# Optimization experiments

Measured on AMD Instinct MI355X. Metric: run time of the kernel, lower is better.

Reference implementation:

```python
import jax, jax.numpy as jnp
import numpy as np

B, P, K, L, F_NR, KS, NC = 32, 2048, 16, 8, 64, 5, 40
N = B * P
EPS = 1e-5


def setup_inputs() -> dict:
    key = jax.random.key(0)
    ks = jax.random.split(key, 6)
    pos = jax.random.normal(ks[0], (N, 3), jnp.float32)
    batch = jnp.repeat(jnp.arange(B, dtype=jnp.int32), P)
    # SplineConv(1, F_NR, dim=3, kernel_size=KS): weight [KS^3, in=1, out] flattened to [KS^3, F]
    w_spline = jax.random.normal(ks[1], (KS ** 3, F_NR), jnp.float32) * 0.1
    w_root = jax.random.normal(ks[2], (F_NR,), jnp.float32) * 0.1
    b_spline = jnp.zeros((F_NR,), jnp.float32)
    bn_gamma = jnp.ones((F_NR,), jnp.float32)
    bn_beta = jnp.zeros((F_NR,), jnp.float32)
    w1 = jax.random.normal(ks[3], (F_NR, 256), jnp.float32) / np.sqrt(F_NR).astype(np.float32)
    b1 = jnp.zeros((256,), jnp.float32)
    w2 = jax.random.normal(ks[4], (256, NC), jnp.float32) / np.sqrt(256).astype(np.float32)
    b2 = jnp.zeros((NC,), jnp.float32)
    return dict(pos=pos, batch=batch, w_spline=w_spline, w_root=w_root,
                b_spline=b_spline, bn_gamma=bn_gamma, bn_beta=bn_beta,
                w1=w1, b1=b1, w2=w2, b2=b2)


def _knn_one_cloud(pb):  # pb: [P,3] -> k nearest neighbor indices [P,K] (no self loops)
    sq = jnp.sum(pb * pb, axis=-1)
    d = sq[:, None] + sq[None, :] - 2.0 * (pb @ pb.T)
    d = jnp.where(jnp.eye(P, dtype=bool), jnp.inf, d)
    _, idx = jax.lax.top_k(-d, K)
    return idx


def reference(pos, batch, w_spline, w_root, b_spline, bn_gamma, bn_beta, w1, b1, w2, b2):
    # --- knn_graph, grouped k-per-center ---
    posb = pos.reshape(B, P, 3)
    nbr = jax.vmap(_knn_one_cloud)(posb)                          # [B,P,K] local
    nbr = (nbr + (jnp.arange(B) * P)[:, None, None]).reshape(N, K)
    clusters = pos[nbr] - pos[:, None, :]                          # [N,K,3]
    # --- per-point 3x3 covariance over first L neighbors ---
    cl = clusters[:, :L, :]
    cov = jnp.einsum('nlc,nld->ncd', cl, cl)                       # [N,3,3]
    # --- diag(): 5 iterations of batched QR iteration; rows of V = eigenvectors ---
    A = cov
    Vt = jnp.broadcast_to(jnp.eye(3, dtype=pos.dtype), (N, 3, 3))
    for _ in range(5):
        Q, R = jnp.linalg.qr(A)
        A = R @ Q
        Vt = Vt @ Q
    V = jnp.swapaxes(Vt, 1, 2)                                     # [N,3,3]
    # --- rotate clusters into eigenbasis: clusters @ V^T ---
    dc = jnp.einsum('nkc,ndc->nkd', clusters, V)                   # [N,K,3]
    signs = jnp.sign(jnp.sum(dc[:, :, 2], axis=1))
    dc = dc.at[:, :, 2].multiply(signs[:, None])
    max_abs = jnp.max(jnp.abs(dc).reshape(N, K * 3), axis=1)
    dc = dc / max_abs[:, None, None] * 0.5 + 0.5                   # pseudo coords in [0,1]
    # --- SplineConv (degree-1 open B-splines, dim=3): x_j = 1, aggr='mean' ---
    p = dc * (KS - 1)
    i0 = jnp.clip(jnp.floor(p), 0, KS - 2).astype(jnp.int32)       # [N,K,3]
    f = p - i0                                                     # fractional part
    acc = jnp.zeros((N, K, F_NR), pos.dtype)
    for c in range(8):                                             # 8 corners of trilinear basis
        bits = [(c >> d) & 1 for d in range(3)]
        kidx = sum((i0[..., d] + bits[d]) * (KS ** d) for d in range(3))
        w = jnp.ones((N, K), pos.dtype)
        for d in range(3):
            w = w * (f[..., d] if bits[d] else 1.0 - f[..., d])
        acc = acc + w[..., None] * w_spline[kidx]                  # [N,K,F]
    out_nondir = acc.mean(axis=1) + w_root + b_spline              # root*x_i + bias, x_i = 1
    # --- BatchNorm1d (training-mode batch stats, biased var) ---
    mu = out_nondir.mean(axis=0)
    var = out_nondir.var(axis=0)
    y = (out_nondir - mu) / jnp.sqrt(var + EPS) * bn_gamma + bn_beta
    # --- head ---
    y = jax.nn.sigmoid(y)
    ys = y.reshape(B, P, F_NR).mean(axis=1)                        # [B,F]
    y1 = jax.nn.elu(ys @ w1 + b1)
    y2 = jax.nn.log_softmax(y1 @ w2 + b2, axis=1)
    return y2
```

## Files before the change

kernel.cpp:

```cpp
#include <hip/hip_runtime.h>
#include <math.h>

#define B_ 32
#define P_ 2048
#define N_ 65536
#define K_ 16
#define L_ 8
#define F_ 64
#define KS_ 5
#define KS3_ 125
#define NC_ 40
#define H_ 256
#define EPS_ 1e-5f
#define QPB_ 64
#define SEG_ 4

__device__ __forceinline__ float distf(float4 C, float nx, float ny, float nz, float qs) {
    return fmaf(C.x, nx, fmaf(C.y, ny, fmaf(C.z, nz, C.w))) + qs;
}

#define CES(a, b) { unsigned _mn = min(a, b); b = max(a, b); a = _mn; }

__device__ __forceinline__ void sort8(unsigned& e0, unsigned& e1, unsigned& e2, unsigned& e3,
                                      unsigned& e4, unsigned& e5, unsigned& e6, unsigned& e7) {
    CES(e0, e1) CES(e2, e3) CES(e4, e5) CES(e6, e7)
    CES(e0, e2) CES(e1, e3) CES(e4, e6) CES(e5, e7)
    CES(e1, e2) CES(e5, e6)
    CES(e0, e4) CES(e1, e5) CES(e2, e6) CES(e3, e7)
    CES(e2, e4) CES(e3, e5)
    CES(e1, e2) CES(e3, e4) CES(e5, e6)
}

__device__ __forceinline__ void bitmerge16(unsigned (&a)[16]) {
#pragma unroll
    for (int dd = 8; dd >= 1; dd >>= 1)
#pragma unroll
        for (int k2 = 0; k2 < 16; k2 += 2 * dd)
#pragma unroll
            for (int i2 = k2; i2 < k2 + dd; i2++)
                CES(a[i2], a[i2 + dd])
}

__device__ __forceinline__ void sort16(unsigned (&a)[16]) {
    sort8(a[0], a[1], a[2], a[3], a[4], a[5], a[6], a[7]);
    sort8(a[8], a[9], a[10], a[11], a[12], a[13], a[14], a[15]);
    unsigned t;
    t = a[8];  a[8]  = a[15]; a[15] = t;
    t = a[9];  a[9]  = a[14]; a[14] = t;
    t = a[10]; a[10] = a[13]; a[13] = t;
    t = a[11]; a[11] = a[12]; a[12] = t;
    bitmerge16(a);
}

__device__ __forceinline__ void flush8(unsigned (&bu)[16],
                                       unsigned& e0, unsigned& e1, unsigned& e2, unsigned& e3,
                                       unsigned& e4, unsigned& e5, unsigned& e6, unsigned& e7,
                                       unsigned& thr) {
    sort8(e0, e1, e2, e3, e4, e5, e6, e7);
    CES(bu[8],  e7) CES(bu[9],  e6) CES(bu[10], e5) CES(bu[11], e4)
    CES(bu[12], e3) CES(bu[13], e2) CES(bu[14], e1) CES(bu[15], e0)
    bitmerge16(bu);
    e0 = e1 = e2 = e3 = e4 = e5 = e6 = e7 = 0xFFFFFFFFu;
    unsigned t16 = bu[15];
    t16 = min(t16, (unsigned)__shfl_xor((int)t16, 1, 64));
    t16 = min(t16, (unsigned)__shfl_xor((int)t16, 2, 64));
    thr = min(thr, t16);
}

__global__ __launch_bounds__(256, 2) void knn_geom_kernel(const float* __restrict__ pos,
                                                          float* __restrict__ dcn) {
    __shared__ float4 cloud[P_ + 8];
    int b = blockIdx.x >> 5, tile = blockIdx.x & 31;
    int base = b * P_;
    int t = threadIdx.x;
    for (int j = t; j < P_; j += 256) {
        float x = pos[(base + j) * 3 + 0];
        float y = pos[(base + j) * 3 + 1];
        float z = pos[(base + j) * 3 + 2];
        cloud[j] = make_float4(x, y, z, x * x + y * y + z * z);
    }
    if (t < 8) cloud[P_ + t] = make_float4(0.f, 0.f, 0.f, 1e30f);
    __syncthreads();

    int s = t & 3;
    int il = tile * QPB_ + (t >> 2);
    float4 Q = cloud[il];
    float nx = -2.f * Q.x, ny = -2.f * Q.y, nz = -2.f * Q.z, qs = Q.w;

    int j0 = s << 9, off = s << 1;

    unsigned bu[16];
#pragma unroll
    for (int m = 0; m < 16; m++) {
        int j_ = j0 + off + m;
        float4 Cv = cloud[j_];
        float d_ = distf(Cv, nx, ny, nz, qs);
        bu[m] = (__float_as_uint(fmaxf(d_, 0.f)) & 0xFFFFF800u) | (unsigned)j_;
    }
    sort16(bu);
    unsigned thr;
    {
        unsigned t16 = bu[15];
        t16 = min(t16, (unsigned)__shfl_xor((int)t16, 1, 64));
        t16 = min(t16, (unsigned)__shfl_xor((int)t16, 2, 64));
        thr = t16;
    }

    unsigned e0 = ~0u, e1 = ~0u, e2 = ~0u, e3 = ~0u,
             e4 = ~0u, e5 = ~0u, e6 = ~0u, e7 = ~0u;

#define VISITL(Cv, Jv) {                                                         \
        float d_ = distf(Cv, nx, ny, nz, qs);                                    \
        unsigned key_ = (__float_as_uint(fmaxf(d_, 0.f)) & 0xFFFFF800u)          \
                        | (unsigned)(Jv);                                        \
        bool a_ = (key_ < thr);                                                  \
        e7 = a_ ? e6 : e7;  e6 = a_ ? e5 : e6;  e5 = a_ ? e4 : e5;               \
        e4 = a_ ? e3 : e4;  e3 = a_ ? e2 : e3;  e2 = a_ ? e1 : e2;               \
        e1 = a_ ? e0 : e1;  e0 = a_ ? key_ : e0;                                 \
    }
#define VISITP(Cv, Jv, P) {                                                      \
        float d_ = distf(Cv, nx, ny, nz, qs);                                    \
        unsigned key_ = (__float_as_uint(fmaxf(d_, 0.f)) & 0xFFFFF800u)          \
                        | (unsigned)(Jv);                                        \
        bool a_ = (key_ < thr) && (P);                                           \
        e7 = a_ ? e6 : e7;  e6 = a_ ? e5 : e6;  e5 = a_ ? e4 : e5;               \
        e4 = a_ ? e3 : e4;  e3 = a_ ? e2 : e3;  e2 = a_ ? e1 : e2;               \
        e1 = a_ ? e0 : e1;  e0 = a_ ? key_ : e0;                                 \
    }

    const float4* cp = &cloud[j0 + off + 16];
    int jc = j0 + off + 16;
    for (int v = 0; v < 488; v += 4) {
        float4 a0 = cp[v + 0], a1 = cp[v + 1], a2 = cp[v + 2], a3 = cp[v + 3];
        VISITL(a0, jc + 0)
        VISITL(a1, jc + 1)
        VISITL(a2, jc + 2)
        VISITL(a3, jc + 3)
        jc += 4;
        if (__any(e4 != 0xFFFFFFFFu))
            flush8(bu, e0, e1, e2, e3, e4, e5, e6, e7, thr);
    }
    {
        int vlim = 496 - off;
#pragma unroll
        for (int v = 488; v < 492; v++) {
            float4 a0 = cp[v];
            VISITP(a0, jc, v < vlim) jc++;
        }
        if (__any(e4 != 0xFFFFFFFFu))
            flush8(bu, e0, e1, e2, e3, e4, e5, e6, e7, thr);
#pragma unroll
        for (int v = 492; v < 496; v++) {
            float4 a0 = cp[v];
            VISITP(a0, jc, v < vlim) jc++;
        }
        if (__any(e4 != 0xFFFFFFFFu))
            flush8(bu, e0, e1, e2, e3, e4, e5, e6, e7, thr);
    }
    {
#pragma unroll
        for (int u = 0; u < 4; u++) {
            float4 a0 = cloud[j0 + u];
            VISITP(a0, j0 + u, u < off)
        }
        if (__any(e4 != 0xFFFFFFFFu))
            flush8(bu, e0, e1, e2, e3, e4, e5, e6, e7, thr);
#pragma unroll
        for (int u = 4; u < 6; u++) {
            float4 a0 = cloud[j0 + u];
            VISITP(a0, j0 + u, u < off)
        }
    }
    flush8(bu, e0, e1, e2, e3, e4, e5, e6, e7, thr);
#undef VISITL
#undef VISITP

    {
        bool own = (s == (il >> 9));
#pragma unroll
        for (int m = 0; m < 15; m++) bu[m] = own ? bu[m + 1] : bu[m];
        bu[15] = own ? 0xFFFFFFFFu : bu[15];
    }

#pragma unroll
    for (int mask = 1; mask <= 2; mask <<= 1) {
        unsigned o[16];
#pragma unroll
        for (int i = 0; i < 16; i++)
            o[i] = (unsigned)__shfl_xor((int)bu[15 - i], mask, 64);
#pragma unroll
        for (int i = 0; i < 16; i++) bu[i] = min(bu[i], o[i]);
        bitmerge16(bu);
    }

    float px = Q.x, py = Q.y, pz = Q.z;
    float A[3][3];
    {
        float a00 = 0, a01 = 0, a02 = 0, a11 = 0, a12 = 0, a22 = 0;
#pragma unroll
        for (int l = 0; l < L_; l++) {
            float4 Cv = cloud[bu[l] & 0x7FF];
            float ccx = Cv.x - px, ccy = Cv.y - py, ccz = Cv.z - pz;
            a00 += ccx * ccx; a01 += ccx * ccy; a02 += ccx * ccz;
            a11 += ccy * ccy; a12 += ccy * ccz; a22 += ccz * ccz;
        }
        A[0][0] = a00; A[0][1] = a01; A[0][2] = a02;
        A[1][0] = a01; A[1][1] = a11; A[1][2] = a12;
        A[2][0] = a02; A[2][1] = a12; A[2][2] = a22;
    }
    float Vt[3][3] = {{1.f, 0.f, 0.f}, {0.f, 1.f, 0.f}, {0.f, 0.f, 1.f}};

    for (int it = 0; it < 5; it++) {
        float M00 = A[0][0], M01 = A[0][1], M02 = A[0][2];
        float M10 = A[1][0], M11 = A[1][1], M12 = A[1][2];
        float M20 = A[2][0], M21 = A[2][1], M22 = A[2][2];
        float tau0 = 0.f, v1 = 0.f, v2 = 0.f;
        float xn2 = M10 * M10 + M20 * M20;
        if (xn2 != 0.f) {
            float beta = -copysignf(sqrtf(M00 * M00 + xn2), M00);
            tau0 = (beta - M00) / beta;
            float inv = 1.f / (M00 - beta);
            v1 = M10 * inv; v2 = M20 * inv;
            float sc;
            sc = tau0 * (M01 + v1 * M11 + v2 * M21); M01 -= sc; M11 -= v1 * sc; M21 -= v2 * sc;
            sc = tau0 * (M02 + v1 * M12 + v2 * M22); M02 -= sc; M12 -= v1 * sc; M22 -= v2 * sc;
            M00 = beta;
        }
        float tau1 = 0.f, u2 = 0.f;
        if (M21 != 0.f) {
            float beta1 = -copysignf(sqrtf(M11 * M11 + M21 * M21), M11);
            tau1 = (beta1 - M11) / beta1;
            u2 = M21 / (M11 - beta1);
            float sc = tau1 * (M12 + u2 * M22); M12 -= sc; M22 -= u2 * sc;
            M11 = beta1;
        }
        float h11 = 1.f - tau1, h12 = -tau1 * u2, h22 = 1.f - tau1 * u2 * u2;
        float Qm[3][3];
        Qm[0][0] = 1.f - tau0;
        Qm[1][0] = -v1 * tau0;
        Qm[2][0] = -v2 * tau0;
        float t1 = tau0 * (v1 * h11 + v2 * h12);
        Qm[0][1] = -t1;
        Qm[1][1] = h11 - v1 * t1;
        Qm[2][1] = h12 - v2 * t1;
        float t2 = tau0 * (v1 * h12 + v2 * h22);
        Qm[0][2] = -t2;
        Qm[1][2] = h12 - v1 * t2;
        Qm[2][2] = h22 - v2 * t2;
        A[0][0] = M00 * Qm[0][0] + M01 * Qm[1][0] + M02 * Qm[2][0];
        A[0][1] = M00 * Qm[0][1] + M01 * Qm[1][1] + M02 * Qm[2][1];
        A[0][2] = M00 * Qm[0][2] + M01 * Qm[1][2] + M02 * Qm[2][2];
        A[1][0] = M11 * Qm[1][0] + M12 * Qm[2][0];
        A[1][1] = M11 * Qm[1][1] + M12 * Qm[2][1];
        A[1][2] = M11 * Qm[1][2] + M12 * Qm[2][2];
        A[2][0] = M22 * Qm[2][0];
        A[2][1] = M22 * Qm[2][1];
        A[2][2] = M22 * Qm[2][2];
        float nv[3][3];
#pragma unroll
        for (int r = 0; r < 3; r++)
#pragma unroll
            for (int cc = 0; cc < 3; cc++)
                nv[r][cc] = Vt[r][0] * Qm[0][cc] + Vt[r][1] * Qm[1][cc] + Vt[r][2] * Qm[2][cc];
#pragma unroll
        for (int r = 0; r < 3; r++)
#pragma unroll
            for (int cc = 0; cc < 3; cc++) Vt[r][cc] = nv[r][cc];
    }

    float s2 = 0.f, mx01 = 0.f, mx2 = 0.f;
#pragma unroll
    for (int k = 0; k < K_; k++) {
        float4 Cv = cloud[bu[k] & 0x7FF];
        float ccx = Cv.x - px, ccy = Cv.y - py, ccz = Cv.z - pz;
        float d0 = ccx * Vt[0][0] + ccy * Vt[1][0] + ccz * Vt[2][0];
        float d1 = ccx * Vt[0][1] + ccy * Vt[1][1] + ccz * Vt[2][1];
        float d2 = ccx * Vt[0][2] + ccy * Vt[1][2] + ccz * Vt[2][2];
        s2 += d2;
        mx01 = fmaxf(mx01, fmaxf(fabsf(d0), fabsf(d1)));
        mx2  = fmaxf(mx2, fabsf(d2));
    }
    float sg = (s2 > 0.f) ? 1.f : ((s2 < 0.f) ? -1.f : 0.f);
    float mx = fmaxf(mx01, (sg == 0.f) ? 0.f : mx2);
    float hs = 0.5f / mx;

    {
        int i = base + il;
        float4* row = (float4*)(dcn + (size_t)i * 48);
        bool od = (s & 1) != 0, hi = (s & 2) != 0;
        unsigned lo0 = od ? bu[4]  : bu[0],  hi0 = od ? bu[12] : bu[8];
        unsigned lo1 = od ? bu[5]  : bu[1],  hi1 = od ? bu[13] : bu[9];
        unsigned lo2 = od ? bu[6]  : bu[2],  hi2 = od ? bu[14] : bu[10];
        unsigned lo3 = od ? bu[7]  : bu[3],  hi3 = od ? bu[15] : bu[11];
        unsigned u0 = hi ? hi0 : lo0;
        unsigned u1 = hi ? hi1 : lo1;
        unsigned u2 = hi ? hi2 : lo2;
        unsigned u3 = hi ? hi3 : lo3;
        float v[12];
        float4 Cv;
        Cv = cloud[u0 & 0x7FF];
        {
            float ccx = Cv.x - px, ccy = Cv.y - py, ccz = Cv.z - pz;
            float d2 = (ccx * Vt[0][2] + ccy * Vt[1][2] + ccz * Vt[2][2]) * sg;
            v[0] = (ccx * Vt[0][0] + ccy * Vt[1][0] + ccz * Vt[2][0]) * hs + 0.5f;
            v[1] = (ccx * Vt[0][1] + ccy * Vt[1][1] + ccz * Vt[2][1]) * hs + 0.5f;
            v[2] = d2 * hs + 0.5f;
        }
        Cv = cloud[u1 & 0x7FF];
        {
            float ccx = Cv.x - px, ccy = Cv.y - py, ccz = Cv.z - pz;
            float d2 = (ccx * Vt[0][2] + ccy * Vt[1][2] + ccz * Vt[2][2]) * sg;
            v[3] = (ccx * Vt[0][0] + ccy * Vt[1][0] + ccz * Vt[2][0]) * hs + 0.5f;
            v[4] = (ccx * Vt[0][1] + ccy * Vt[1][1] + ccz * Vt[2][1]) * hs + 0.5f;
            v[5] = d2 * hs + 0.5f;
        }
        Cv = cloud[u2 & 0x7FF];
        {
            float ccx = Cv.x - px, ccy = Cv.y - py, ccz = Cv.z - pz;
            float d2 = (ccx * Vt[0][2] + ccy * Vt[1][2] + ccz * Vt[2][2]) * sg;
            v[6] = (ccx * Vt[0][0] + ccy * Vt[1][0] + ccz * Vt[2][0]) * hs + 0.5f;
            v[7] = (ccx * Vt[0][1] + ccy * Vt[1][1] + ccz * Vt[2][1]) * hs + 0.5f;
            v[8] = d2 * hs + 0.5f;
        }
        Cv = cloud[u3 & 0x7FF];
        {
            float ccx = Cv.x - px, ccy = Cv.y - py, ccz = Cv.z - pz;
            float d2 = (ccx * Vt[0][2] + ccy * Vt[1][2] + ccz * Vt[2][2]) * sg;
            v[9]  = (ccx * Vt[0][0] + ccy * Vt[1][0] + ccz * Vt[2][0]) * hs + 0.5f;
            v[10] = (ccx * Vt[0][1] + ccy * Vt[1][1] + ccz * Vt[2][1]) * hs + 0.5f;
            v[11] = d2 * hs + 0.5f;
        }
        row[s * 3 + 0] = make_float4(v[0], v[1], v[2], v[3]);
        row[s * 3 + 1] = make_float4(v[4], v[5], v[6], v[7]);
        row[s * 3 + 2] = make_float4(v[8], v[9], v[10], v[11]);
    }
}

__global__ __launch_bounds__(256) void spline_kernel(const float* __restrict__ dcn,
                                                     const float* __restrict__ w_spline,
                                                     const float* __restrict__ w_root,
                                                     const float* __restrict__ b_spline,
                                                     float* __restrict__ x,
                                                     float* __restrict__ partials) {
    __shared__ float ws_t[F_ * KS3_];
    __shared__ float red[4][64];
    {
        int f = threadIdx.x & 63;
        for (int c = threadIdx.x >> 6; c < KS3_; c += 4)
            ws_t[f * KS3_ + c] = w_spline[c * 64 + f];
    }
    __syncthreads();
    int wave = threadIdx.x >> 6, f = threadIdx.x & 63;
    const float* wbase = &ws_t[f * KS3_];
    float wr = w_root[f] + b_spline[f];
    float s1 = 0.f, s2 = 0.f;
    for (int p = 0; p < 16; p++) {
        int i = blockIdx.x * 64 + wave * 16 + p;
        const float4* row = (const float4*)(dcn + (size_t)i * 48);
        float pr[48];
#pragma unroll
        for (int m = 0; m < 12; m++) {
            float4 v = row[m];
            pr[m * 4 + 0] = v.x; pr[m * 4 + 1] = v.y;
            pr[m * 4 + 2] = v.z; pr[m * 4 + 3] = v.w;
        }
        float acc = 0.f;
#pragma unroll
        for (int k = 0; k < K_; k++) {
            float p0 = pr[k * 3 + 0] * 4.f;
            float p1 = pr[k * 3 + 1] * 4.f;
            float p2 = pr[k * 3 + 2] * 4.f;
            float i0 = fminf(fmaxf(floorf(p0), 0.f), 3.f);
            float i1 = fminf(fmaxf(floorf(p1), 0.f), 3.f);
            float i2 = fminf(fmaxf(floorf(p2), 0.f), 3.f);
            float f0 = p0 - i0, f1 = p1 - i1, f2 = p2 - i2;
            float g0 = 1.f - f0, g1 = 1.f - f1, g2 = 1.f - f2;
            int c = (int)fmaf(i2, 25.f, fmaf(i1, 5.f, i0));
            const float* wp = wbase + c;
            float a0 = wp[0],  a1 = wp[1];
            float b0 = wp[5],  b1v = wp[6];
            float c0 = wp[25], c1 = wp[26];
            float d0 = wp[30], d1 = wp[31];
            float wA = g1 * g2, wB = f1 * g2, wC = g1 * f2, wD = f1 * f2;
            acc = fmaf(wA, fmaf(f0, a1, g0 * a0), acc);
            acc = fmaf(wB, fmaf(f0, b1v, g0 * b0), acc);
            acc = fmaf(wC, fmaf(f0, c1, g0 * c0), acc);
            acc = fmaf(wD, fmaf(f0, d1, g0 * d0), acc);
        }
        float xv = acc * (1.f / 16.f) + wr;
        x[(size_t)i * 64 + f] = xv;
        s1 += xv; s2 += xv * xv;
    }
    red[wave][f] = s1; __syncthreads();
    if (threadIdx.x < 64)
        partials[blockIdx.x * 128 + f] = red[0][f] + red[1][f] + red[2][f] + red[3][f];
    __syncthreads();
    red[wave][f] = s2; __syncthreads();
    if (threadIdx.x < 64)
        partials[blockIdx.x * 128 + 64 + f] = red[0][f] + red[1][f] + red[2][f] + red[3][f];
}

__global__ __launch_bounds__(256) void stats_kernel(const float* __restrict__ partials,
                                                    const float* __restrict__ gamma,
                                                    const float* __restrict__ beta,
                                                    float* __restrict__ stats) {
    __shared__ double red1[256], red2[256];
    int t = threadIdx.x;
    int f = t & 63, g = t >> 6;
    double a0 = 0, a1 = 0, a2 = 0, a3 = 0, q0 = 0, q1 = 0, q2 = 0, q3 = 0;
    for (int b2 = g; b2 < 1024; b2 += 16) {
        a0 += (double)partials[(b2     ) * 128 + f];
        q0 += (double)partials[(b2     ) * 128 + 64 + f];
        a1 += (double)partials[(b2 +  4) * 128 + f];
        q1 += (double)partials[(b2 +  4) * 128 + 64 + f];
        a2 += (double)partials[(b2 +  8) * 128 + f];
        q2 += (double)partials[(b2 +  8) * 128 + 64 + f];
        a3 += (double)partials[(b2 + 12) * 128 + f];
        q3 += (double)partials[(b2 + 12) * 128 + 64 + f];
    }
    red1[t] = (a0 + a1) + (a2 + a3);
    red2[t] = (q0 + q1) + (q2 + q3);
    __syncthreads();
    if (t < 64) {
        double S1 = red1[t] + red1[t + 64] + red1[t + 128] + red1[t + 192];
        double S2 = red2[t] + red2[t + 64] + red2[t + 128] + red2[t + 192];
        double mu = S1 / (double)N_;
        double var = S2 / (double)N_ - mu * mu;
        double scale = (double)gamma[t] / sqrt(var + (double)EPS_);
        double shift = (double)beta[t] - mu * scale;
        stats[t] = (float)scale;
        stats[64 + t] = (float)shift;
    }
}

__global__ __launch_bounds__(256) void pool_partial_kernel(const float* __restrict__ x,
                                                           const float* __restrict__ stats,
                                                           float* __restrict__ pp) {
    __shared__ float red[4][64];
    int blk = blockIdx.x;
    int b = blk >> 5, ch = blk & 31;
    int f = threadIdx.x & 63, w = threadIdx.x >> 6;
    float scale = stats[f], shift = stats[64 + f];
    float acc = 0.f;
    int row0 = b * P_ + ch * 64;
    for (int r = w; r < 64; r += 4) {
        float v = x[(size_t)(row0 + r) * 64 + f];
        float t = fmaf(v, scale, shift);
        acc += __fdividef(1.f, 1.f + __expf(-t));
    }
    red[w][f] = acc; __syncthreads();
    if (threadIdx.x < 64) pp[blk * 64 + f] = red[0][f] + red[1][f] + red[2][f] + red[3][f];
}

__global__ __launch_bounds__(256) void mlp_kernel(const float* __restrict__ pp,
                                                  const float* __restrict__ w1,
                                                  const float* __restrict__ b1,
                                                  const float* __restrict__ w2,
                                                  const float* __restrict__ b2,
                                                  float* __restrict__ out) {
    __shared__ float ssy[64];
    __shared__ float sy1[256];
    int b = blockIdx.x, t = threadIdx.x;
    if (t < 64) {
        float s = 0.f;
#pragma unroll
        for (int g = 0; g < 32; g++) s += pp[(b * 32 + g) * 64 + t];
        ssy[t] = s * (1.f / 2048.f);
    }
    __syncthreads();
    {
        float acc = b1[t];
#pragma unroll 8
        for (int c = 0; c < F_; c++) acc = fmaf(ssy[c], w1[c * 256 + t], acc);
        sy1[t] = acc > 0.f ? acc : expm1f(acc);
    }
    __syncthreads();
    if (t < 64) {
        int j = t;
        float acc = -INFINITY;
        if (j < NC_) {
            acc = b2[j];
#pragma unroll 8
            for (int c = 0; c < H_; c++) acc = fmaf(sy1[c], w2[c * 40 + j], acc);
        }
        float m = acc;
#pragma unroll
        for (int o = 32; o > 0; o >>= 1) m = fmaxf(m, __shfl_xor(m, o, 64));
        float e = (j < NC_) ? expf(acc - m) : 0.f;
        float s = e;
#pragma unroll
        for (int o = 32; o > 0; o >>= 1) s += __shfl_xor(s, o, 64);
        if (j < NC_) out[b * NC_ + j] = acc - m - logf(s);
    }
}

extern "C" void kernel_launch(void* const* d_in, const int* in_sizes, int n_in,
                              void* d_out, int out_size, void* d_ws, size_t ws_size,
                              hipStream_t stream) {
    const float* pos      = (const float*)d_in[0];
    const float* w_spline = (const float*)d_in[2];
    const float* w_root   = (const float*)d_in[3];
    const float* b_spline = (const float*)d_in[4];
    const float* bn_gamma = (const float*)d_in[5];
    const float* bn_beta  = (const float*)d_in[6];
    const float* w1       = (const float*)d_in[7];
    const float* b1       = (const float*)d_in[8];
    const float* w2       = (const float*)d_in[9];
    const float* b2       = (const float*)d_in[10];
    float* out = (float*)d_out;

    char* ws = (char*)d_ws;
    float* dcn      = (float*)(ws + 0);
    float* x        = (float*)(ws + (12u << 20));
    float* partials = (float*)(ws + (28u << 20));
    float* stats    = (float*)(ws + (28u << 20) + (512u << 10));
    float* pp       = (float*)(ws + (28u << 20) + (512u << 10) + 4096);

    knn_geom_kernel<<<B_ * 32, 256, 0, stream>>>(pos, dcn);
    spline_kernel<<<N_ / 64, 256, 0, stream>>>(dcn, w_spline, w_root, b_spline, x, partials);
    stats_kernel<<<1, 256, 0, stream>>>(partials, bn_gamma, bn_beta, stats);
    pool_partial_kernel<<<B_ * 32, 256, 0, stream>>>(x, stats, pp);
    mlp_kernel<<<B_, 256, 0, stream>>>(pp, w1, b1, w2, b2, out);
}
```

Measured before the change: 194.1 us.

## Store spline weight corners pre-expanded as fp16 for single vector LDS load

The spline kernel now stages, for each feature and each of the 64 base cells, the 8 trilinear corner weights contiguously in shared memory as fp16. Each neighbor then needs one 16-byte LDS read instead of eight scalar reads. The interpolation is refactored to nested lerps and the clamp uses fmed3. This trades fp16 precision on the weights for fewer LDS instructions, and the expanded table uses about 66KB of shared memory, which may lower occupancy.

After: 218.6 us. 1.13x slower.

```diff
diff --git a/kernel.cpp b/kernel.cpp
--- a/kernel.cpp
+++ b/kernel.cpp
@@ -1,4 +1,5 @@
 #include <hip/hip_runtime.h>
+#include <hip/hip_fp16.h>
 #include <math.h>
 
 #define B_ 32
@@ -342,16 +343,22 @@
                                                      const float* __restrict__ b_spline,
                                                      float* __restrict__ x,
                                                      float* __restrict__ partials) {
-    __shared__ float ws_t[F_ * KS3_];
+    __shared__ __half exp_h[F_ * 520];
     __shared__ float red[4][64];
-    {
-        int f = threadIdx.x & 63;
-        for (int c = threadIdx.x >> 6; c < KS3_; c += 4)
-            ws_t[f * KS3_ + c] = w_spline[c * 64 + f];
+    for (int idx = threadIdx.x; idx < 64 * 64; idx += 256) {
+        int f = idx & 63, bb = idx >> 6;
+        int i0 = bb & 3, i1 = (bb >> 2) & 3, i2 = bb >> 4;
+        const float* wp = w_spline + (i0 + 5 * i1 + 25 * i2) * 64 + f;
+        __half2 h0 = __float22half2_rn(make_float2(wp[0 * 64],  wp[1 * 64]));
+        __half2 h1 = __float22half2_rn(make_float2(wp[5 * 64],  wp[6 * 64]));
+        __half2 h2 = __float22half2_rn(make_float2(wp[25 * 64], wp[26 * 64]));
+        __half2 h3 = __float22half2_rn(make_float2(wp[30 * 64], wp[31 * 64]));
+        __half2* dst = (__half2*)&exp_h[f * 520 + bb * 8];
+        dst[0] = h0; dst[1] = h1; dst[2] = h2; dst[3] = h3;
     }
     __syncthreads();
     int wave = threadIdx.x >> 6, f = threadIdx.x & 63;
-    const float* wbase = &ws_t[f * KS3_];
+    const __half* exp_row = &exp_h[f * 520];
     float wr = w_root[f] + b_spline[f];
     float s1 = 0.f, s2 = 0.f;
     for (int p = 0; p < 16; p++) {
@@ -370,22 +377,25 @@
             float p0 = pr[k * 3 + 0] * 4.f;
             float p1 = pr[k * 3 + 1] * 4.f;
             float p2 = pr[k * 3 + 2] * 4.f;
-            float i0 = fminf(fmaxf(floorf(p0), 0.f), 3.f);
-            float i1 = fminf(fmaxf(floorf(p1), 0.f), 3.f);
-            float i2 = fminf(fmaxf(floorf(p2), 0.f), 3.f);
+            float i0 = __builtin_amdgcn_fmed3f(floorf(p0), 0.f, 3.f);
+            float i1 = __builtin_amdgcn_fmed3f(floorf(p1), 0.f, 3.f);
+            float i2 = __builtin_amdgcn_fmed3f(floorf(p2), 0.f, 3.f);
             float f0 = p0 - i0, f1 = p1 - i1, f2 = p2 - i2;
             float g0 = 1.f - f0, g1 = 1.f - f1, g2 = 1.f - f2;
-            int c = (int)fmaf(i2, 25.f, fmaf(i1, 5.f, i0));
-            const float* wp = wbase + c;
-            float a0 = wp[0],  a1 = wp[1];
-            float b0 = wp[5],  b1v = wp[6];
-            float c0 = wp[25], c1 = wp[26];
-            float d0 = wp[30], d1 = wp[31];
-            float wA = g1 * g2, wB = f1 * g2, wC = g1 * f2, wD = f1 * f2;
-            acc = fmaf(wA, fmaf(f0, a1, g0 * a0), acc);
-            acc = fmaf(wB, fmaf(f0, b1v, g0 * b0), acc);
-            acc = fmaf(wC, fmaf(f0, c1, g0 * c0), acc);
-            acc = fmaf(wD, fmaf(f0, d1, g0 * d0), acc);
+            int bb = (int)fmaf(i2, 16.f, fmaf(i1, 4.f, i0));
+            uint4 rv = *((const uint4*)(exp_row + bb * 8));
+            float2 cA = __half22float2(*(__half2*)&rv.x);
+            float2 cB = __half22float2(*(__half2*)&rv.y);
+            float2 cC = __half22float2(*(__half2*)&rv.z);
+            float2 cD = __half22float2(*(__half2*)&rv.w);
+            float Av = fmaf(f0, cA.y, g0 * cA.x);
+            float Bv = fmaf(f0, cB.y, g0 * cB.x);
+            float Cv = fmaf(f0, cC.y, g0 * cC.x);
+            float Dv = fmaf(f0, cD.y, g0 * cD.x);
+            float U = fmaf(f1, Bv, g1 * Av);
+            float V = fmaf(f1, Dv, g1 * Cv);
+            acc = fmaf(g2, U, acc);
+            acc = fmaf(f2, V, acc);
         }
         float xv = acc * (1.f / 16.f) + wr;
         x[(size_t)i * 64 + f] = xv;
```

## Restructure spline conv as scatter to dense coefficients then fp16 dot2 matmul

Applied to the files above, without the earlier changes.

The spline kernel now builds, per point, a dense 125-entry trilinear coefficient vector in shared memory by atomically accumulating the 8 corner weights of each of the 16 neighbours. That vector is packed to fp16 and multiplied against fp16-packed spline weights held in registers using dot2 instructions. This replaces the per-feature, per-neighbour gather and interpolation loop, which repeated the interpolation weights across all 64 features. In exchange it adds fp16 rounding of both weights and coefficients, LDS atomics, a large register array for the weights, and drops the lower clamp on the floor index.

Result: slower. 204.2 us (+5.2%).

```diff
diff --git a/kernel.cpp b/kernel.cpp
--- a/kernel.cpp
+++ b/kernel.cpp
@@ -14,6 +14,23 @@
 #define EPS_ 1e-5f
 #define QPB_ 64
 #define SEG_ 4
+
+typedef _Float16 h2v __attribute__((ext_vector_type(2)));
+
+__device__ __forceinline__ h2v u2h(unsigned u) { h2v h; __builtin_memcpy(&h, &u, 4); return h; }
+
+__device__ __forceinline__ unsigned pkrtz(float a, float b) {
+    auto h = __builtin_amdgcn_cvt_pkrtz(a, b);
+    unsigned u; __builtin_memcpy(&u, &h, 4); return u;
+}
+
+#if __has_builtin(__builtin_amdgcn_fdot2)
+#define DOT2(a, b, c) __builtin_amdgcn_fdot2((a), (b), (c), false)
+#else
+__device__ __forceinline__ float DOT2(h2v a, h2v b, float c) {
+    return fmaf((float)a[0], (float)b[0], fmaf((float)a[1], (float)b[1], c));
+}
+#endif
 
 __device__ __forceinline__ float distf(float4 C, float nx, float ny, float nz, float qs) {
     return fmaf(C.x, nx, fmaf(C.y, ny, fmaf(C.z, nz, C.w))) + qs;
@@ -342,62 +359,114 @@
                                                      const float* __restrict__ b_spline,
                                                      float* __restrict__ x,
                                                      float* __restrict__ partials) {
-    __shared__ float ws_t[F_ * KS3_];
+    __shared__ float C32[64 * 128];
+    __shared__ unsigned Wt2[64 * 64];
     __shared__ float red[4][64];
-    {
-        int f = threadIdx.x & 63;
-        for (int c = threadIdx.x >> 6; c < KS3_; c += 4)
-            ws_t[f * KS3_ + c] = w_spline[c * 64 + f];
-    }
-    __syncthreads();
-    int wave = threadIdx.x >> 6, f = threadIdx.x & 63;
-    const float* wbase = &ws_t[f * KS3_];
-    float wr = w_root[f] + b_spline[f];
-    float s1 = 0.f, s2 = 0.f;
-    for (int p = 0; p < 16; p++) {
-        int i = blockIdx.x * 64 + wave * 16 + p;
-        const float4* row = (const float4*)(dcn + (size_t)i * 48);
-        float pr[48];
-#pragma unroll
-        for (int m = 0; m < 12; m++) {
-            float4 v = row[m];
-            pr[m * 4 + 0] = v.x; pr[m * 4 + 1] = v.y;
-            pr[m * 4 + 2] = v.z; pr[m * 4 + 3] = v.w;
-        }
-        float acc = 0.f;
-#pragma unroll
-        for (int k = 0; k < K_; k++) {
-            float p0 = pr[k * 3 + 0] * 4.f;
-            float p1 = pr[k * 3 + 1] * 4.f;
-            float p2 = pr[k * 3 + 2] * 4.f;
-            float i0 = fminf(fmaxf(floorf(p0), 0.f), 3.f);
-            float i1 = fminf(fmaxf(floorf(p1), 0.f), 3.f);
-            float i2 = fminf(fmaxf(floorf(p2), 0.f), 3.f);
+    int t = threadIdx.x;
+    int base_i = blockIdx.x * 64;
+
+    {
+        float4 z = make_float4(0.f, 0.f, 0.f, 0.f);
+        float4* c4 = (float4*)C32;
+#pragma unroll
+        for (int r = 0; r < 8; r++) c4[t + r * 256] = z;
+    }
+    for (int idx = t; idx < 64 * 64; idx += 256) {
+        int f = idx & 63, cc = idx >> 6;
+        float w0 = (2 * cc < KS3_) ? w_spline[(2 * cc) * 64 + f] : 0.f;
+        float w1 = (2 * cc + 1 < KS3_) ? w_spline[(2 * cc + 1) * 64 + f] : 0.f;
+        Wt2[idx] = pkrtz(w0, w1);
+    }
+    __syncthreads();
+
+    {
+        int p = t & 63, kg = t >> 6;
+        const float4* dr = (const float4*)(dcn + (size_t)(base_i + p) * 48) + kg * 3;
+        float4 fa = dr[0], fb = dr[1], fc = dr[2];
+        float* crow = &C32[p * 128];
+        float sx[12] = {fa.x, fa.y, fa.z, fa.w, fb.x, fb.y, fb.z, fb.w, fc.x, fc.y, fc.z, fc.w};
+#pragma unroll
+        for (int q = 0; q < 4; q++) {
+            float p0 = sx[q * 3 + 0] * 4.f;
+            float p1 = sx[q * 3 + 1] * 4.f;
+            float p2 = sx[q * 3 + 2] * 4.f;
+            float i0 = fminf(floorf(p0), 3.f);
+            float i1 = fminf(floorf(p1), 3.f);
+            float i2 = fminf(floorf(p2), 3.f);
             float f0 = p0 - i0, f1 = p1 - i1, f2 = p2 - i2;
             float g0 = 1.f - f0, g1 = 1.f - f1, g2 = 1.f - f2;
             int c = (int)fmaf(i2, 25.f, fmaf(i1, 5.f, i0));
-            const float* wp = wbase + c;
-            float a0 = wp[0],  a1 = wp[1];
-            float b0 = wp[5],  b1v = wp[6];
-            float c0 = wp[25], c1 = wp[26];
-            float d0 = wp[30], d1 = wp[31];
             float wA = g1 * g2, wB = f1 * g2, wC = g1 * f2, wD = f1 * f2;
-            acc = fmaf(wA, fmaf(f0, a1, g0 * a0), acc);
-            acc = fmaf(wB, fmaf(f0, b1v, g0 * b0), acc);
-            acc = fmaf(wC, fmaf(f0, c1, g0 * c0), acc);
-            acc = fmaf(wD, fmaf(f0, d1, g0 * d0), acc);
-        }
-        float xv = acc * (1.f / 16.f) + wr;
-        x[(size_t)i * 64 + f] = xv;
-        s1 += xv; s2 += xv * xv;
-    }
-    red[wave][f] = s1; __syncthreads();
-    if (threadIdx.x < 64)
-        partials[blockIdx.x * 128 + f] = red[0][f] + red[1][f] + red[2][f] + red[3][f];
-    __syncthreads();
-    red[wave][f] = s2; __syncthreads();
-    if (threadIdx.x < 64)
-        partials[blockIdx.x * 128 + 64 + f] = red[0][f] + red[1][f] + red[2][f] + red[3][f];
+            atomicAdd(&crow[c + 0],  g0 * wA);
+            atomicAdd(&crow[c + 1],  f0 * wA);
+            atomicAdd(&crow[c + 5],  g0 * wB);
+            atomicAdd(&crow[c + 6],  f0 * wB);
+            atomicAdd(&crow[c + 25], g0 * wC);
+            atomicAdd(&crow[c + 26], f0 * wC);
+            atomicAdd(&crow[c + 30], g0 * wD);
+            atomicAdd(&crow[c + 31], f0 * wD);
+        }
+    }
+    __syncthreads();
+
+    float st[32];
+    {
+        int p = t >> 2, w4 = t & 3;
+        const float4* src = (const float4*)&C32[p * 128] + w4 * 8;
+#pragma unroll
+        for (int r = 0; r < 8; r++) {
+            float4 v = src[r];
+            st[r * 4 + 0] = v.x; st[r * 4 + 1] = v.y;
+            st[r * 4 + 2] = v.z; st[r * 4 + 3] = v.w;
+        }
+    }
+    __syncthreads();
+    {
+        int p = t >> 2, w4 = t & 3;
+        uint4* dst = (uint4*)C32 + p * 16 + w4 * 4;
+#pragma unroll
+        for (int r = 0; r < 4; r++) {
+            uint4 pk;
+            pk.x = pkrtz(st[r * 8 + 0], st[r * 8 + 1]);
+            pk.y = pkrtz(st[r * 8 + 2], st[r * 8 + 3]);
+            pk.z = pkrtz(st[r * 8 + 4], st[r * 8 + 5]);
+            pk.w = pkrtz(st[r * 8 + 6], st[r * 8 + 7]);
+            dst[r] = pk;
+        }
+    }
+    __syncthreads();
+
+    {
+        int wave = t >> 6, f = t & 63;
+        float wr = w_root[f] + b_spline[f];
+        h2v wreg[64];
+#pragma unroll
+        for (int cc = 0; cc < 64; cc++) wreg[cc] = u2h(Wt2[cc * 64 + f]);
+        const uint4* C16q = (const uint4*)C32;
+        float s1 = 0.f, s2sum = 0.f;
+        for (int pp = 0; pp < 16; pp++) {
+            int p = wave * 16 + pp;
+            float a0 = 0.f, a1 = 0.f, a2 = 0.f, a3 = 0.f;
+#pragma unroll
+            for (int ch = 0; ch < 16; ch++) {
+                uint4 rv = C16q[p * 16 + ch];
+                a0 = DOT2(u2h(rv.x), wreg[ch * 4 + 0], a0);
+                a1 = DOT2(u2h(rv.y), wreg[ch * 4 + 1], a1);
+                a2 = DOT2(u2h(rv.z), wreg[ch * 4 + 2], a2);
+                a3 = DOT2(u2h(rv.w), wreg[ch * 4 + 3], a3);
+            }
+            float xv = ((a0 + a1) + (a2 + a3)) * (1.f / 16.f) + wr;
+            x[(size_t)(base_i + p) * 64 + f] = xv;
+            s1 += xv; s2sum += xv * xv;
+        }
+        red[wave][f] = s1; __syncthreads();
+        if (t < 64)
+            partials[blockIdx.x * 128 + f] = red[0][f] + red[1][f] + red[2][f] + red[3][f];
+        __syncthreads();
+        red[wave][f] = s2sum; __syncthreads();
+        if (t < 64)
+            partials[blockIdx.x * 128 + 64 + f] = red[0][f] + red[1][f] + red[2][f] + red[3][f];
+    }
 }
 
 __global__ __launch_bounds__(256) void stats_kernel(const float* __restrict__ partials,
```
